# Kernel tuning notes

Measured on AMD Instinct MI355X. Metric: run time of the kernel, lower is better.

## Reference

```python
import jax, jax.numpy as jnp
import numpy as np

B, HID, NV = 2, 128, 16
H, W = 361, 720
PAD = 2          # bicubic padding
A = -0.75        # torch grid_sample bicubic coefficient


def _pole_fix(x):
    # force single scalar value at each pole row (mean over longitude)
    s = x[:, :, 0:1, :].mean(axis=3, keepdims=True)
    n = x[:, :, -1:, :].mean(axis=3, keepdims=True)
    x = x.at[:, :, 0:1, :].set(jnp.broadcast_to(s, x[:, :, 0:1, :].shape))
    x = x.at[:, :, -1:, :].set(jnp.broadcast_to(n, x[:, :, -1:, :].shape))
    return x


def _geo_pad(x, p):
    # geo-cyclic padding: pole rows reflected with half-world longitude shift,
    # longitude padded cyclically
    Wd = x.shape[-1]
    top = jnp.roll(jnp.flip(x[:, :, :p, :], axis=2), Wd // 2, axis=3)
    bot = jnp.roll(jnp.flip(x[:, :, -p:, :], axis=2), Wd // 2, axis=3)
    x = jnp.concatenate([top, x, bot], axis=2)
    return jnp.concatenate([x[:, :, :, -p:], x, x[:, :, :, :p]], axis=3)


def _cubic_w(t):
    # cubic convolution weights (a = -0.75), matches torch bicubic
    t1 = t + 1.0
    t2 = 1.0 - t
    t3 = 2.0 - t
    w0 = ((A * t1 - 5.0 * A) * t1 + 8.0 * A) * t1 - 4.0 * A
    w1 = ((A + 2.0) * t - (A + 3.0)) * t * t + 1.0
    w2 = ((A + 2.0) * t2 - (A + 3.0)) * t2 * t2 + 1.0
    w3 = ((A * t3 - 5.0 * A) * t3 + 8.0 * A) * t3 - 4.0 * A
    return (w0, w1, w2, w3)


def _bicubic_sample(img, ix, iy):
    # img: [N, Hp, Wp]; ix, iy: [N, h, w] pixel coords (align_corners=True),
    # padding_mode='zeros' => out-of-bounds taps contribute zero
    N, Hp, Wp = img.shape
    x0f = jnp.floor(ix)
    y0f = jnp.floor(iy)
    tx = ix - x0f
    ty = iy - y0f
    x0 = x0f.astype(jnp.int32)
    y0 = y0f.astype(jnp.int32)
    wx = _cubic_w(tx)
    wy = _cubic_w(ty)
    flat = img.reshape(N, Hp * Wp)
    out = jnp.zeros_like(ix)
    for dy in range(4):
        yy = y0 + (dy - 1)
        vy = (yy >= 0) & (yy < Hp)
        yyc = jnp.clip(yy, 0, Hp - 1)
        for dx in range(4):
            xx = x0 + (dx - 1)
            vx = (xx >= 0) & (xx < Wp)
            xxc = jnp.clip(xx, 0, Wp - 1)
            lin = (yyc * Wp + xxc).reshape(N, -1)
            val = jnp.take_along_axis(flat, lin, axis=1).reshape(ix.shape)
            out = out + val * (wy[dy] * wx[dx] * (vy & vx).astype(img.dtype))
    return out


def _forward(hidden_features, u, v, dt, lat_grid, lon_grid,
             down_w, down_b, dw_w, dw_b, up_w, up_b):
    Bc, C, Hc, Wc = hidden_features.shape
    min_lat, max_lat = lat_grid.min(), lat_grid.max()
    min_lon, max_lon = lon_grid.min(), lon_grid.max()
    d_lat = max_lat - min_lat
    d_lon = max_lon - min_lon

    x = _pole_fix(hidden_features)
    # down projection: 1x1 CLinear hidden_dim -> num_vels
    proj = jnp.einsum('bchw,oc->bohw', x, down_w) + down_b[None, :, None, None]

    # departure point in rotated coords
    lon_pr = -u * dt
    lat_pr = -v * dt
    lat_g = lat_grid[None, None]  # [1,1,H,W]
    lon_g = lon_grid[None, None]
    sin_lat_pr, cos_lat_pr = jnp.sin(lat_pr), jnp.cos(lat_pr)
    sin_lon_pr, cos_lon_pr = jnp.sin(lon_pr), jnp.cos(lon_pr)
    sin_lat_g, cos_lat_g = jnp.sin(lat_g), jnp.cos(lat_g)
    sin_lat = sin_lat_pr * cos_lat_g + cos_lat_pr * cos_lon_pr * sin_lat_g
    lat_dep = jnp.arcsin(jnp.clip(sin_lat, -1.0 + 1e-7, 1.0 - 1e-7))
    num = cos_lat_pr * sin_lon_pr
    den = cos_lat_pr * cos_lon_pr * cos_lat_g - sin_lat_pr * sin_lat_g
    lon_dep = lon_g + jnp.arctan2(num, den)
    lon_dep = jnp.remainder(lon_dep + 2.0 * jnp.pi, 2.0 * jnp.pi)

    pix_x = (lon_dep - min_lon) / d_lon * (Wc - 1.0)
    pix_y = (lat_dep - min_lat) / d_lat * (Hc - 1.0)
    Hp, Wp = Hc + 2 * PAD, Wc + 2 * PAD
    # normalize then unnormalize (align_corners=True) as in torch path
    grid_x = 2.0 * ((pix_x + PAD) / float(Wp - 1)) - 1.0
    grid_y = 2.0 * ((pix_y + PAD) / float(Hp - 1)) - 1.0
    ix = (grid_x + 1.0) * 0.5 * (Wp - 1)
    iy = (grid_y + 1.0) * 0.5 * (Hp - 1)

    padded = _geo_pad(proj, PAD).reshape(Bc * NV, Hp, Wp)
    ix = ix.reshape(Bc * NV, Hc, Wc)
    iy = iy.reshape(Bc * NV, Hc, Wc)
    interp = _bicubic_sample(padded, ix, iy).reshape(Bc, NV, Hc, Wc)

    # up projection: SepConv k=1 -> depthwise 1x1 then pointwise 1x1
    y = interp * dw_w[None, :, None, None] + dw_b[None, :, None, None]
    out = jnp.einsum('bvhw,ov->bohw', y, up_w) + up_b[None, :, None, None]
    return _pole_fix(out)


def setup_inputs() -> dict:
    key = jax.random.key(0)
    k = jax.random.split(key, 6)
    lat = jnp.linspace(-jnp.pi / 2, jnp.pi / 2, H, dtype=jnp.float32)
    lon = jnp.arange(W, dtype=jnp.float32) * jnp.float32(2.0 * np.pi / W)
    lon_grid, lat_grid = jnp.meshgrid(lon, lat)  # [H, W] each
    return {
        'hidden_features': jax.random.normal(k[0], (B, HID, H, W), jnp.float32),
        'u': jax.random.normal(k[1], (B, NV, H, W), jnp.float32) * 0.01,
        'v': jax.random.normal(k[2], (B, NV, H, W), jnp.float32) * 0.01,
        'dt': jnp.float32(1.0),
        'lat_grid': lat_grid.astype(jnp.float32),
        'lon_grid': lon_grid.astype(jnp.float32),
        'down_w': jax.random.normal(k[3], (NV, HID), jnp.float32) / np.float32(np.sqrt(HID)),
        'down_b': jnp.zeros((NV,), jnp.float32),
        'dw_w': jax.random.normal(k[4], (NV,), jnp.float32),
        'dw_b': jnp.zeros((NV,), jnp.float32),
        'up_w': jax.random.normal(k[5], (HID, NV), jnp.float32) / np.float32(np.sqrt(NV)),
        'up_b': jnp.zeros((HID,), jnp.float32),
    }


def reference(hidden_features, u, v, dt, lat_grid, lon_grid,
              down_w, down_b, dw_w, dw_b, up_w, up_b):
    return _forward(hidden_features, u, v, dt, lat_grid, lon_grid,
                    down_w, down_b, dw_w, dw_b, up_w, up_b)
```

## Files before the change

kernel.cpp:

```cpp
#include <hip/hip_runtime.h>
#include <math.h>

#define B_    2
#define HID_  128
#define NV_   16
#define H_    361
#define W_    720
#define PAD_  2
#define HP_   (H_ + 2*PAD_)
#define WP_   (W_ + 2*PAD_)
#define HW_   (H_ * W_)
#define PIX_  (B_ * H_ * W_)
#define TWO_PI_ 6.2831853071795864769f

__global__ __launch_bounds__(256) void k_down(const float* __restrict__ hid,
                                              const float* __restrict__ dwn_w,
                                              const float* __restrict__ dwn_b,
                                              float* __restrict__ proj)
{
    __shared__ float wt[HID_ * NV_];
    for (int i = threadIdx.x; i < HID_ * NV_; i += 256) {
        int v = i >> 7;
        int c = i & 127;
        wt[c * NV_ + v] = dwn_w[i];
    }
    __syncthreads();

    int chunk = blockIdx.x * 256 + threadIdx.x;
    int pix0 = chunk * 4;
    if (pix0 >= PIX_) return;
    int b  = pix0 / HW_;
    int hw = pix0 - b * HW_;

    const float* src = hid + (size_t)b * HID_ * HW_ + hw;

    float acc[NV_][4];
    #pragma unroll
    for (int v = 0; v < NV_; ++v) {
        float bv = dwn_b[v];
        acc[v][0] = bv; acc[v][1] = bv; acc[v][2] = bv; acc[v][3] = bv;
    }

    for (int c = 0; c < HID_; ++c) {
        float4 x = *(const float4*)(src + (size_t)c * HW_);
        const float4* wr = (const float4*)(&wt[c * NV_]);
        float4 w4[4];
        w4[0] = wr[0]; w4[1] = wr[1]; w4[2] = wr[2]; w4[3] = wr[3];
        const float* wsc = (const float*)w4;
        #pragma unroll
        for (int v = 0; v < NV_; ++v) {
            float wv = wsc[v];
            acc[v][0] = fmaf(x.x, wv, acc[v][0]);
            acc[v][1] = fmaf(x.y, wv, acc[v][1]);
            acc[v][2] = fmaf(x.z, wv, acc[v][2]);
            acc[v][3] = fmaf(x.w, wv, acc[v][3]);
        }
    }

    float* dst = proj + (size_t)b * NV_ * HW_ + hw;
    #pragma unroll
    for (int v = 0; v < NV_; ++v) {
        *(float4*)(dst + (size_t)v * HW_) =
            make_float4(acc[v][0], acc[v][1], acc[v][2], acc[v][3]);
    }
}

__global__ __launch_bounds__(256) void k_polefix(float* __restrict__ x)
{
    int ch  = blockIdx.x >> 1;
    int row = (blockIdx.x & 1) ? (H_ - 1) : 0;
    float* rowp = x + (size_t)ch * HW_ + (size_t)row * W_;

    float s = 0.f;
    for (int w = threadIdx.x; w < W_; w += 256) s += rowp[w];
    #pragma unroll
    for (int off = 32; off > 0; off >>= 1) s += __shfl_down(s, off, 64);
    __shared__ float wpart[4];
    if ((threadIdx.x & 63) == 0) wpart[threadIdx.x >> 6] = s;
    __syncthreads();
    float total = wpart[0] + wpart[1] + wpart[2] + wpart[3];
    float mean = total / 720.0f;
    for (int w = threadIdx.x; w < W_; w += 256) rowp[w] = mean;
}

__device__ __forceinline__ float psin(float x) {
    float x2 = x * x;
    return x * fmaf(x2, fmaf(x2, 1.f/120.f, -1.f/6.f), 1.f);
}
__device__ __forceinline__ float pcos(float x) {
    float x2 = x * x;
    return fmaf(x2, fmaf(x2, fmaf(x2, -1.f/720.f, 1.f/24.f), -0.5f), 1.f);
}

__device__ __forceinline__ float fasinf(float x) {
    float ax = fabsf(x);
    float p = fmaf(ax, -0.0012624911f, 0.0066700901f);
    p = fmaf(ax, p, -0.0170881256f);
    p = fmaf(ax, p,  0.0308918810f);
    p = fmaf(ax, p, -0.0501743046f);
    p = fmaf(ax, p,  0.0889789874f);
    p = fmaf(ax, p, -0.2145988016f);
    p = fmaf(ax, p,  1.5707963050f);
    float r = 1.5707963268f - sqrtf(1.f - ax) * p;
    return copysignf(r, x);
}

__device__ __forceinline__ float fatan2f(float y, float x) {
    float ax = fabsf(x), ay = fabsf(y);
    float mx = fmaxf(ax, ay), mn = fminf(ax, ay);
    float t  = mn * __builtin_amdgcn_rcpf(fmaxf(mx, 1e-38f));
    float t2 = t * t;
    float p = fmaf(t2, -0.0117212f,  0.05265332f);
    p = fmaf(t2, p, -0.11643287f);
    p = fmaf(t2, p,  0.19354346f);
    p = fmaf(t2, p, -0.33262347f);
    p = fmaf(t2, p,  0.99997726f);
    float r = t * p;
    r = (ay > ax) ? 1.5707963268f - r : r;
    r = (x < 0.f) ? 3.1415926536f - r : r;
    return copysignf(r, y);
}

__device__ __forceinline__ void cubw(float t, float w[4]) {
    const float Ac = -0.75f;
    float t1 = t + 1.f, t2 = 1.f - t, t3 = 2.f - t;
    w[0] = ((Ac*t1 - 5.f*Ac)*t1 + 8.f*Ac)*t1 - 4.f*Ac;
    w[1] = ((Ac + 2.f)*t  - (Ac + 3.f))*t*t   + 1.f;
    w[2] = ((Ac + 2.f)*t2 - (Ac + 3.f))*t2*t2 + 1.f;
    w[3] = ((Ac*t3 - 5.f*Ac)*t3 + 8.f*Ac)*t3 - 4.f*Ac;
}

__global__ __launch_bounds__(256) void k_adv(const float* __restrict__ proj,
                                             const float* __restrict__ uu,
                                             const float* __restrict__ vvv,
                                             const float* __restrict__ dtp,
                                             const float* __restrict__ latg,
                                             const float* __restrict__ lon_p,
                                             const float* __restrict__ dw_w,
                                             const float* __restrict__ dw_b,
                                             const float* __restrict__ up_w,
                                             const float* __restrict__ up_b,
                                             float* __restrict__ out)
{
    int pix = blockIdx.x * 256 + threadIdx.x;
    if (pix >= PIX_) return;
    int b  = pix / HW_;
    int hw = pix - b * HW_;

    float dt = dtp[0];
    float min_lat = latg[0];
    float max_lat = latg[(size_t)(H_ - 1) * W_];
    float min_lon = lon_p[0];
    float max_lon = lon_p[W_ - 1];
    float sx = (float)(W_ - 1) / (max_lon - min_lon);
    float sy = (float)(H_ - 1) / (max_lat - min_lat);

    float lat_gv = latg[hw];
    float slg, clg;
    sincosf(lat_gv, &slg, &clg);
    float lon_g = lon_p[hw];

    const float* pvb = proj + (size_t)b * NV_ * HW_;
    float y[NV_];

    for (int v = 0; v < NV_; ++v) {
        size_t vbase = (size_t)(b * NV_ + v) * HW_ + hw;
        float uval = __builtin_nontemporal_load(uu  + vbase);
        float vval = __builtin_nontemporal_load(vvv + vbase);
        const float* pv = pvb + (size_t)v * HW_;

        float lon_pr = -uval * dt;
        float lat_pr = -vval * dt;
        float slp = psin(lat_pr), clp = pcos(lat_pr);
        float slo = psin(lon_pr), clo = pcos(lon_pr);

        float sin_lat = slp * clg + clp * clo * slg;
        sin_lat = fminf(fmaxf(sin_lat, -1.f + 1e-7f), 1.f - 1e-7f);
        float lat_dep = fasinf(sin_lat);
        float num = clp * slo;
        float den = clp * clo * clg - slp * slg;
        float lon_dep = lon_g + fatan2f(num, den);
        lon_dep = (lon_dep <  0.f)     ? lon_dep + TWO_PI_ : lon_dep;
        lon_dep = (lon_dep >= TWO_PI_) ? lon_dep - TWO_PI_ : lon_dep;

        float ix = fmaf(lon_dep - min_lon, sx, (float)PAD_);
        float iy = fmaf(lat_dep - min_lat, sy, (float)PAD_);

        float x0f = floorf(ix), y0f = floorf(iy);
        float tx = ix - x0f, ty = iy - y0f;
        int x0 = (int)x0f, y0 = (int)y0f;
        float wx[4], wy[4];
        cubw(tx, wx);
        cubw(ty, wy);

        float s = 0.f;
        if (y0 >= 3 && y0 <= 360 && x0 >= 3 && x0 <= 719) {
            const float* tp = pv + (size_t)((y0 - 3) * W_ + (x0 - 3));
            #pragma unroll
            for (int dy = 0; dy < 4; ++dy) {
                const float* rp = tp + (size_t)dy * W_;
                float rs =      rp[0] * wx[0];
                rs = fmaf(rp[1], wx[1], rs);
                rs = fmaf(rp[2], wx[2], rs);
                rs = fmaf(rp[3], wx[3], rs);
                s = fmaf(rs, wy[dy], s);
            }
        } else {
            #pragma unroll
            for (int dy = 0; dy < 4; ++dy) {
                int yy = y0 + dy - 1;
                if (yy < 0 || yy >= HP_) continue;
                int rr, shift;
                if (yy < PAD_)            { rr = PAD_ - 1 - yy;             shift = PAD_ + W_/2; }
                else if (yy >= PAD_ + H_) { rr = H_ - 1 - (yy - PAD_ - H_); shift = PAD_ + W_/2; }
                else                      { rr = yy - PAD_;                 shift = PAD_; }
                const float* rowp = pv + (size_t)rr * W_;
                float rs = 0.f;
                #pragma unroll
                for (int dx = 0; dx < 4; ++dx) {
                    int xx = x0 + dx - 1;
                    if (xx < 0 || xx >= WP_) continue;
                    int cc = xx - shift;
                    if (cc < 0)    cc += W_;
                    if (cc >= W_)  cc -= W_;
                    rs = fmaf(rowp[cc], wx[dx], rs);
                }
                s = fmaf(rs, wy[dy], s);
            }
        }
        y[v] = fmaf(s, dw_w[v], dw_b[v]);
    }

    float* obase = out + (size_t)b * HID_ * HW_ + hw;
    for (int o = 0; o < HID_; ++o) {
        const float4* wr = (const float4*)(up_w + o * NV_);
        float4 wa = wr[0], wb = wr[1], wc = wr[2], wd = wr[3];
        float a = up_b[o];
        a = fmaf(y[0],  wa.x, a); a = fmaf(y[1],  wa.y, a);
        a = fmaf(y[2],  wa.z, a); a = fmaf(y[3],  wa.w, a);
        a = fmaf(y[4],  wb.x, a); a = fmaf(y[5],  wb.y, a);
        a = fmaf(y[6],  wb.z, a); a = fmaf(y[7],  wb.w, a);
        a = fmaf(y[8],  wc.x, a); a = fmaf(y[9],  wc.y, a);
        a = fmaf(y[10], wc.z, a); a = fmaf(y[11], wc.w, a);
        a = fmaf(y[12], wd.x, a); a = fmaf(y[13], wd.y, a);
        a = fmaf(y[14], wd.z, a); a = fmaf(y[15], wd.w, a);
        __builtin_nontemporal_store(a, obase + (size_t)o * HW_);
    }
}

extern "C" void kernel_launch(void* const* d_in, const int* in_sizes, int n_in,
                              void* d_out, int out_size, void* d_ws, size_t ws_size,
                              hipStream_t stream)
{
    const float* hid   = (const float*)d_in[0];
    const float* u     = (const float*)d_in[1];
    const float* v     = (const float*)d_in[2];
    const float* dt    = (const float*)d_in[3];
    const float* latg  = (const float*)d_in[4];
    const float* lon_p = (const float*)d_in[5];
    const float* dwn_w = (const float*)d_in[6];
    const float* dwn_b = (const float*)d_in[7];
    const float* dw_w  = (const float*)d_in[8];
    const float* dw_b  = (const float*)d_in[9];
    const float* up_w  = (const float*)d_in[10];
    const float* up_b  = (const float*)d_in[11];
    float* out  = (float*)d_out;
    float* proj = (float*)d_ws;

    int nchunks = PIX_ / 4;
    int blocks4 = (nchunks + 255) / 256;
    int blocks1 = (PIX_ + 255) / 256;

    hipLaunchKernelGGL(k_down, dim3(blocks4), dim3(256), 0, stream,
                       hid, dwn_w, dwn_b, proj);
    hipLaunchKernelGGL(k_polefix, dim3(B_ * NV_ * 2), dim3(256), 0, stream, proj);
    hipLaunchKernelGGL(k_adv, dim3(blocks1), dim3(256), 0, stream,
                       proj, u, v, dt, latg, lon_p, dw_w, dw_b, up_w, up_b, out);
    hipLaunchKernelGGL(k_polefix, dim3(B_ * HID_ * 2), dim3(256), 0, stream, out);
}
```

Measured before the change: 643.2 us.

## Split advection into separate sampling and up-projection kernels via workspace

Splits the fused advect-and-project kernel into k_samp, which writes the 16 sampled channels to a workspace buffer, and k_up, which does the 128-channel up-projection on two pixels per thread. It also halves k_down's per-thread pixel count from four to two and prefetches the next u/v values inside the sampling loop. The goal is to relieve register pressure and the long serial per-thread work of the fused kernel, raising occupancy and memory-level parallelism. The cost is an extra launch plus a write and re-read of a 16-channel intermediate, and the split path only runs when the workspace holds two projection buffers.

```diff
diff --git a/kernel.cpp b/kernel.cpp
--- a/kernel.cpp
+++ b/kernel.cpp
@@ -12,6 +12,7 @@
 #define HW_   (H_ * W_)
 #define PIX_  (B_ * H_ * W_)
 #define TWO_PI_ 6.2831853071795864769f
+#define PROJ_BYTES_ ((size_t)B_ * NV_ * HW_ * 4)
 
 __global__ __launch_bounds__(256) void k_down(const float* __restrict__ hid,
                                               const float* __restrict__ dwn_w,
@@ -27,22 +28,22 @@
     __syncthreads();
 
     int chunk = blockIdx.x * 256 + threadIdx.x;
-    int pix0 = chunk * 4;
+    int pix0 = chunk * 2;
     if (pix0 >= PIX_) return;
     int b  = pix0 / HW_;
     int hw = pix0 - b * HW_;
 
     const float* src = hid + (size_t)b * HID_ * HW_ + hw;
 
-    float acc[NV_][4];
+    float acc[NV_][2];
     #pragma unroll
     for (int v = 0; v < NV_; ++v) {
         float bv = dwn_b[v];
-        acc[v][0] = bv; acc[v][1] = bv; acc[v][2] = bv; acc[v][3] = bv;
+        acc[v][0] = bv; acc[v][1] = bv;
     }
 
     for (int c = 0; c < HID_; ++c) {
-        float4 x = *(const float4*)(src + (size_t)c * HW_);
+        float2 x = *(const float2*)(src + (size_t)c * HW_);
         const float4* wr = (const float4*)(&wt[c * NV_]);
         float4 w4[4];
         w4[0] = wr[0]; w4[1] = wr[1]; w4[2] = wr[2]; w4[3] = wr[3];
@@ -52,16 +53,13 @@
             float wv = wsc[v];
             acc[v][0] = fmaf(x.x, wv, acc[v][0]);
             acc[v][1] = fmaf(x.y, wv, acc[v][1]);
-            acc[v][2] = fmaf(x.z, wv, acc[v][2]);
-            acc[v][3] = fmaf(x.w, wv, acc[v][3]);
         }
     }
 
     float* dst = proj + (size_t)b * NV_ * HW_ + hw;
     #pragma unroll
     for (int v = 0; v < NV_; ++v) {
-        *(float4*)(dst + (size_t)v * HW_) =
-            make_float4(acc[v][0], acc[v][1], acc[v][2], acc[v][3]);
+        *(float2*)(dst + (size_t)v * HW_) = make_float2(acc[v][0], acc[v][1]);
     }
 }
 
@@ -130,6 +128,166 @@
     w[3] = ((Ac*t3 - 5.f*Ac)*t3 + 8.f*Ac)*t3 - 4.f*Ac;
 }
 
+__device__ __forceinline__ float sample_one(const float* __restrict__ pv,
+                                            float uval, float vval, float dt,
+                                            float slg, float clg, float lon_g,
+                                            float min_lat, float min_lon,
+                                            float sx, float sy)
+{
+    float lon_pr = -uval * dt;
+    float lat_pr = -vval * dt;
+    float slp = psin(lat_pr), clp = pcos(lat_pr);
+    float slo = psin(lon_pr), clo = pcos(lon_pr);
+
+    float sin_lat = slp * clg + clp * clo * slg;
+    sin_lat = fminf(fmaxf(sin_lat, -1.f + 1e-7f), 1.f - 1e-7f);
+    float lat_dep = fasinf(sin_lat);
+    float num = clp * slo;
+    float den = clp * clo * clg - slp * slg;
+    float lon_dep = lon_g + fatan2f(num, den);
+    lon_dep = (lon_dep <  0.f)     ? lon_dep + TWO_PI_ : lon_dep;
+    lon_dep = (lon_dep >= TWO_PI_) ? lon_dep - TWO_PI_ : lon_dep;
+
+    float ix = fmaf(lon_dep - min_lon, sx, (float)PAD_);
+    float iy = fmaf(lat_dep - min_lat, sy, (float)PAD_);
+
+    float x0f = floorf(ix), y0f = floorf(iy);
+    float tx = ix - x0f, ty = iy - y0f;
+    int x0 = (int)x0f, y0 = (int)y0f;
+    float wx[4], wy[4];
+    cubw(tx, wx);
+    cubw(ty, wy);
+
+    float s = 0.f;
+    if (y0 >= 3 && y0 <= 360 && x0 >= 3 && x0 <= 719) {
+        const float* tp = pv + (size_t)((y0 - 3) * W_ + (x0 - 3));
+        #pragma unroll
+        for (int dy = 0; dy < 4; ++dy) {
+            const float* rp = tp + (size_t)dy * W_;
+            float rs =      rp[0] * wx[0];
+            rs = fmaf(rp[1], wx[1], rs);
+            rs = fmaf(rp[2], wx[2], rs);
+            rs = fmaf(rp[3], wx[3], rs);
+            s = fmaf(rs, wy[dy], s);
+        }
+    } else {
+        #pragma unroll
+        for (int dy = 0; dy < 4; ++dy) {
+            int yy = y0 + dy - 1;
+            if (yy < 0 || yy >= HP_) continue;
+            int rr, shift;
+            if (yy < PAD_)            { rr = PAD_ - 1 - yy;             shift = PAD_ + W_/2; }
+            else if (yy >= PAD_ + H_) { rr = H_ - 1 - (yy - PAD_ - H_); shift = PAD_ + W_/2; }
+            else                      { rr = yy - PAD_;                 shift = PAD_; }
+            const float* rowp = pv + (size_t)rr * W_;
+            float rs = 0.f;
+            #pragma unroll
+            for (int dx = 0; dx < 4; ++dx) {
+                int xx = x0 + dx - 1;
+                if (xx < 0 || xx >= WP_) continue;
+                int cc = xx - shift;
+                if (cc < 0)    cc += W_;
+                if (cc >= W_)  cc -= W_;
+                rs = fmaf(rowp[cc], wx[dx], rs);
+            }
+            s = fmaf(rs, wy[dy], s);
+        }
+    }
+    return s;
+}
+
+__global__ __launch_bounds__(256) void k_samp(const float* __restrict__ proj,
+                                              const float* __restrict__ uu,
+                                              const float* __restrict__ vvv,
+                                              const float* __restrict__ dtp,
+                                              const float* __restrict__ latg,
+                                              const float* __restrict__ lon_p,
+                                              const float* __restrict__ dw_w,
+                                              const float* __restrict__ dw_b,
+                                              float* __restrict__ yout)
+{
+    int pix = blockIdx.x * 256 + threadIdx.x;
+    if (pix >= PIX_) return;
+    int b  = pix / HW_;
+    int hw = pix - b * HW_;
+
+    float dt = dtp[0];
+    float min_lat = latg[0];
+    float max_lat = latg[(size_t)(H_ - 1) * W_];
+    float min_lon = lon_p[0];
+    float max_lon = lon_p[W_ - 1];
+    float sx = (float)(W_ - 1) / (max_lon - min_lon);
+    float sy = (float)(H_ - 1) / (max_lat - min_lat);
+
+    float lat_gv = latg[hw];
+    float slg, clg;
+    sincosf(lat_gv, &slg, &clg);
+    float lon_g = lon_p[hw];
+
+    const float* pvb = proj + (size_t)b * NV_ * HW_;
+    size_t base = (size_t)b * NV_ * HW_ + hw;
+
+    float un = __builtin_nontemporal_load(uu  + base);
+    float vn = __builtin_nontemporal_load(vvv + base);
+
+    for (int v = 0; v < NV_; ++v) {
+        float ucur = un, vcur = vn;
+        if (v + 1 < NV_) {
+            un = __builtin_nontemporal_load(uu  + base + (size_t)(v + 1) * HW_);
+            vn = __builtin_nontemporal_load(vvv + base + (size_t)(v + 1) * HW_);
+        }
+        float s = sample_one(pvb + (size_t)v * HW_, ucur, vcur, dt,
+                             slg, clg, lon_g, min_lat, min_lon, sx, sy);
+        float yv = fmaf(s, dw_w[v], dw_b[v]);
+        __builtin_nontemporal_store(yv, yout + base + (size_t)v * HW_);
+    }
+}
+
+__global__ __launch_bounds__(256) void k_up(const float* __restrict__ yin,
+                                            const float* __restrict__ up_w,
+                                            const float* __restrict__ up_b,
+                                            float* __restrict__ out)
+{
+    int chunk = blockIdx.x * 256 + threadIdx.x;
+    int pix0 = chunk * 2;
+    if (pix0 >= PIX_) return;
+    int b  = pix0 / HW_;
+    int hw = pix0 - b * HW_;
+
+    const float* ybase = yin + (size_t)b * NV_ * HW_ + hw;
+    float y[NV_][2];
+    #pragma unroll
+    for (int v = 0; v < NV_; ++v) {
+        float2 t = *(const float2*)(ybase + (size_t)v * HW_);
+        y[v][0] = t.x; y[v][1] = t.y;
+    }
+
+    float* obase = out + (size_t)b * HID_ * HW_ + hw;
+    for (int o = 0; o < HID_; ++o) {
+        const float4* wr = (const float4*)(up_w + o * NV_);
+        float4 wa = wr[0], wb = wr[1], wc = wr[2], wd = wr[3];
+        float bo = up_b[o];
+        float a0 = bo, a1 = bo;
+        a0 = fmaf(y[0][0],  wa.x, a0); a1 = fmaf(y[0][1],  wa.x, a1);
+        a0 = fmaf(y[1][0],  wa.y, a0); a1 = fmaf(y[1][1],  wa.y, a1);
+        a0 = fmaf(y[2][0],  wa.z, a0); a1 = fmaf(y[2][1],  wa.z, a1);
+        a0 = fmaf(y[3][0],  wa.w, a0); a1 = fmaf(y[3][1],  wa.w, a1);
+        a0 = fmaf(y[4][0],  wb.x, a0); a1 = fmaf(y[4][1],  wb.x, a1);
+        a0 = fmaf(y[5][0],  wb.y, a0); a1 = fmaf(y[5][1],  wb.y, a1);
+        a0 = fmaf(y[6][0],  wb.z, a0); a1 = fmaf(y[6][1],  wb.z, a1);
+        a0 = fmaf(y[7][0],  wb.w, a0); a1 = fmaf(y[7][1],  wb.w, a1);
+        a0 = fmaf(y[8][0],  wc.x, a0); a1 = fmaf(y[8][1],  wc.x, a1);
+        a0 = fmaf(y[9][0],  wc.y, a0); a1 = fmaf(y[9][1],  wc.y, a1);
+        a0 = fmaf(y[10][0], wc.z, a0); a1 = fmaf(y[10][1], wc.z, a1);
+        a0 = fmaf(y[11][0], wc.w, a0); a1 = fmaf(y[11][1], wc.w, a1);
+        a0 = fmaf(y[12][0], wd.x, a0); a1 = fmaf(y[12][1], wd.x, a1);
+        a0 = fmaf(y[13][0], wd.y, a0); a1 = fmaf(y[13][1], wd.y, a1);
+        a0 = fmaf(y[14][0], wd.z, a0); a1 = fmaf(y[14][1], wd.z, a1);
+        a0 = fmaf(y[15][0], wd.w, a0); a1 = fmaf(y[15][1], wd.w, a1);
+        *(float2*)(obase + (size_t)o * HW_) = make_float2(a0, a1);
+    }
+}
+
 __global__ __launch_bounds__(256) void k_adv(const float* __restrict__ proj,
                                              const float* __restrict__ uu,
                                              const float* __restrict__ vvv,
@@ -161,73 +319,14 @@
     float lon_g = lon_p[hw];
 
     const float* pvb = proj + (size_t)b * NV_ * HW_;
+    size_t base = (size_t)b * NV_ * HW_ + hw;
     float y[NV_];
 
     for (int v = 0; v < NV_; ++v) {
-        size_t vbase = (size_t)(b * NV_ + v) * HW_ + hw;
-        float uval = __builtin_nontemporal_load(uu  + vbase);
-        float vval = __builtin_nontemporal_load(vvv + vbase);
-        const float* pv = pvb + (size_t)v * HW_;
-
-        float lon_pr = -uval * dt;
-        float lat_pr = -vval * dt;
-        float slp = psin(lat_pr), clp = pcos(lat_pr);
-        float slo = psin(lon_pr), clo = pcos(lon_pr);
-
-        float sin_lat = slp * clg + clp * clo * slg;
-        sin_lat = fminf(fmaxf(sin_lat, -1.f + 1e-7f), 1.f - 1e-7f);
-        float lat_dep = fasinf(sin_lat);
-        float num = clp * slo;
-        float den = clp * clo * clg - slp * slg;
-        float lon_dep = lon_g + fatan2f(num, den);
-        lon_dep = (lon_dep <  0.f)     ? lon_dep + TWO_PI_ : lon_dep;
-        lon_dep = (lon_dep >= TWO_PI_) ? lon_dep - TWO_PI_ : lon_dep;
-
-        float ix = fmaf(lon_dep - min_lon, sx, (float)PAD_);
-        float iy = fmaf(lat_dep - min_lat, sy, (float)PAD_);
-
-        float x0f = floorf(ix), y0f = floorf(iy);
-        float tx = ix - x0f, ty = iy - y0f;
-        int x0 = (int)x0f, y0 = (int)y0f;
-        float wx[4], wy[4];
-        cubw(tx, wx);
-        cubw(ty, wy);
-
-        float s = 0.f;
-        if (y0 >= 3 && y0 <= 360 && x0 >= 3 && x0 <= 719) {
-            const float* tp = pv + (size_t)((y0 - 3) * W_ + (x0 - 3));
-            #pragma unroll
-            for (int dy = 0; dy < 4; ++dy) {
-                const float* rp = tp + (size_t)dy * W_;
-                float rs =      rp[0] * wx[0];
-                rs = fmaf(rp[1], wx[1], rs);
-                rs = fmaf(rp[2], wx[2], rs);
-                rs = fmaf(rp[3], wx[3], rs);
-                s = fmaf(rs, wy[dy], s);
-            }
-        } else {
-            #pragma unroll
-            for (int dy = 0; dy < 4; ++dy) {
-                int yy = y0 + dy - 1;
-                if (yy < 0 || yy >= HP_) continue;
-                int rr, shift;
-                if (yy < PAD_)            { rr = PAD_ - 1 - yy;             shift = PAD_ + W_/2; }
-                else if (yy >= PAD_ + H_) { rr = H_ - 1 - (yy - PAD_ - H_); shift = PAD_ + W_/2; }
-                else                      { rr = yy - PAD_;                 shift = PAD_; }
-                const float* rowp = pv + (size_t)rr * W_;
-                float rs = 0.f;
-                #pragma unroll
-                for (int dx = 0; dx < 4; ++dx) {
-                    int xx = x0 + dx - 1;
-                    if (xx < 0 || xx >= WP_) continue;
-                    int cc = xx - shift;
-                    if (cc < 0)    cc += W_;
-                    if (cc >= W_)  cc -= W_;
-                    rs = fmaf(rowp[cc], wx[dx], rs);
-                }
-                s = fmaf(rs, wy[dy], s);
-            }
-        }
+        float uval = __builtin_nontemporal_load(uu  + base + (size_t)v * HW_);
+        float vval = __builtin_nontemporal_load(vvv + base + (size_t)v * HW_);
+        float s = sample_one(pvb + (size_t)v * HW_, uval, vval, dt,
+                             slg, clg, lon_g, min_lat, min_lon, sx, sy);
         y[v] = fmaf(s, dw_w[v], dw_b[v]);
     }
 
@@ -267,14 +366,22 @@
     float* out  = (float*)d_out;
     float* proj = (float*)d_ws;
 
-    int nchunks = PIX_ / 4;
-    int blocks4 = (nchunks + 255) / 256;
+    int blocks2 = (PIX_ / 2 + 255) / 256;
     int blocks1 = (PIX_ + 255) / 256;
 
-    hipLaunchKernelGGL(k_down, dim3(blocks4), dim3(256), 0, stream,
+    hipLaunchKernelGGL(k_down, dim3(blocks2), dim3(256), 0, stream,
                        hid, dwn_w, dwn_b, proj);
     hipLaunchKernelGGL(k_polefix, dim3(B_ * NV_ * 2), dim3(256), 0, stream, proj);
-    hipLaunchKernelGGL(k_adv, dim3(blocks1), dim3(256), 0, stream,
-                       proj, u, v, dt, latg, lon_p, dw_w, dw_b, up_w, up_b, out);
+
+    if (ws_size >= 2 * PROJ_BYTES_) {
+        float* ybuf = (float*)((char*)d_ws + PROJ_BYTES_);
+        hipLaunchKernelGGL(k_samp, dim3(blocks1), dim3(256), 0, stream,
+                           proj, u, v, dt, latg, lon_p, dw_w, dw_b, ybuf);
+        hipLaunchKernelGGL(k_up, dim3(blocks2), dim3(256), 0, stream,
+                           ybuf, up_w, up_b, out);
+    } else {
+        hipLaunchKernelGGL(k_adv, dim3(blocks1), dim3(256), 0, stream,
+                           proj, u, v, dt, latg, lon_p, dw_w, dw_b, up_w, up_b, out);
+    }
     hipLaunchKernelGGL(k_polefix, dim3(B_ * HID_ * 2), dim3(256), 0, stream, out);
 }
```

Result: slower. 662.7 us (+3.0%).
